# Kernel optimization log

Hardware: AMD Instinct MI355X
Metric: run time of the kernel (lower is better)

Reference implementation:

```python
import jax, jax.numpy as jnp
import numpy as np

ORDER = 2  # kernel_size


def setup_inputs() -> dict:
    key = jax.random.key(0)
    ks = jax.random.split(key, 8)
    B, F, N, T, H = 8, 1, 1024, 128, 64
    c_in = (ORDER * 2 + 1) * (2 * F + H)  # 330
    x = jax.random.normal(ks[0], (B, F, N, T), jnp.float32)
    mask = jax.random.randint(ks[1], (B, F, N, T), 0, 2).astype(jnp.bool_)
    adj = jax.random.uniform(ks[2], (N, N), jnp.float32)
    Wr = jax.random.normal(ks[3], (H, c_in), jnp.float32) * 0.05
    Wu = jax.random.normal(ks[4], (H, c_in), jnp.float32) * 0.05
    Wc = jax.random.normal(ks[5], (H, c_in), jnp.float32) * 0.05
    Wout = jax.random.normal(ks[6], (F, H), jnp.float32) * 0.05
    return {"x": x, "mask": mask, "adj": adj,
            "Wr": Wr, "br": jnp.zeros((H,), jnp.float32),
            "Wu": Wu, "bu": jnp.zeros((H,), jnp.float32),
            "Wc": Wc, "bc": jnp.zeros((H,), jnp.float32),
            "Wout": Wout, "bout": jnp.zeros((F,), jnp.float32)}


def reference(x, mask, adj, Wr, br, Wu, bu, Wc, bc, Wout, bout):
    # compute_support: forward/backward row-normalized diffusion matrices
    sup_f = adj / (adj.sum(1, keepdims=True) + 1e-8)
    adj_t = adj.T
    sup_b = adj_t / (adj_t.sum(1, keepdims=True) + 1e-8)
    supports = (sup_f, sup_b)

    def sconv(z, W, b):  # SpatialConvOrderK, z: [B,C,N]
        outs = [z]
        for a in supports:
            z1 = z
            for _ in range(ORDER):
                z1 = jnp.einsum('bcv,wv->bcw', z1, a)
                outs.append(z1)
        zc = jnp.concatenate(outs, axis=1)  # [B, 5*C, N]
        return jnp.einsum('bcn,oc->bon', zc, W) + b[None, :, None]

    def cell(inp, h):  # GCGRUCell
        xh = jnp.concatenate([inp, h], axis=1)
        r = jax.nn.sigmoid(sconv(xh, Wr, br))
        u = jax.nn.sigmoid(sconv(xh, Wu, bu))
        c = jnp.tanh(sconv(jnp.concatenate([inp, r * h], axis=1), Wc, bc))
        return u * h + (1.0 - u) * c

    B, F, N, T = x.shape
    H = Wout.shape[1]
    h0 = jnp.zeros((B, H, N), x.dtype)  # n_nodes=None -> zero init
    xs = jnp.moveaxis(x, -1, 0)    # [T,B,F,N]
    ms = jnp.moveaxis(mask, -1, 0)

    def step(h, xm):
        x_s, m_s = xm
        x_hat = jnp.einsum('bhn,oh->bon', h, Wout) + bout[None, :, None]
        state = h[None]  # n_layers=1 -> [L,B,H,N]
        x_in = jnp.where(m_s, x_s, x_hat)
        inp = jnp.concatenate([x_in, m_s.astype(x_s.dtype)], axis=1)
        return cell(inp, h), (x_hat, state)

    _, (preds, states) = jax.lax.scan(step, h0, (xs, ms))
    predictions = jnp.moveaxis(preds, 0, -1)  # [B,F,N,T]
    states = jnp.moveaxis(states, 0, -1)      # [L,B,H,N,T]
    return predictions, states
```

## Files before the change

kernel.cpp:

```cpp
#include <hip/hip_runtime.h>
#include <math.h>


typedef unsigned short u16;
typedef unsigned int u32;
typedef short bf16x8 __attribute__((ext_vector_type(8)));
typedef float f32x4 __attribute__((ext_vector_type(4)));

#define MFMA16(a, b, c) __builtin_amdgcn_mfma_f32_16x16x32_bf16((a), (b), (c), 0, 0, 0)

#define Bz 8
#define Tt 128
#define Hh 64
#define KC 416
#define KL 424
#define CP 148
#define ZLB (32 * KL * 2)
#define SCRB (4 * 64 * 44 * 4)

static __device__ __forceinline__ u16 f2b(float f) {
  u32 u = __float_as_uint(f);
  u = (u + 0x7FFFu + ((u >> 16) & 1u)) >> 16;
  return (u16)u;
}
static __device__ __forceinline__ float b2f(u16 s) { return __uint_as_float(((u32)s) << 16); }
static __device__ __forceinline__ bf16x8 ld8(const u16* p) { return *reinterpret_cast<const bf16x8*>(p); }
static __device__ __forceinline__ void st2f(u16* p, float a, float b) {
  *reinterpret_cast<u32*>(p) = (u32)f2b(a) | ((u32)f2b(b) << 16);
}
static __device__ __forceinline__ float sigm(float x) { return 1.f / (1.f + __expf(-x)); }
static __device__ __forceinline__ float tanh_f(float x) {
  x = fminf(fmaxf(x, -15.f), 15.f);
  float e = __expf(2.f * x);
  return (e - 1.f) / (e + 1.f);
}

__global__ __launch_bounds__(256) void ksums(const float* adj, float* rinv, float* cinv) {
  int id = blockIdx.x * 256 + threadIdx.x;
  if (id < 1024) {
    int w = id;
    float s = 0.f;
    for (int v = 0; v < 1024; ++v) s += adj[v * 1024 + w];
    cinv[w] = 1.f / (s + 1e-8f);
  } else {
    int w = id - 1024;
    float s = 0.f;
    for (int v = 0; v < 1024; ++v) s += adj[w * 1024 + v];
    rinv[w] = 1.f / (s + 1e-8f);
  }
}

__global__ __launch_bounds__(256) void kmakeops(const float* adj, const float* rinv, const float* cinv,
                                                u16* Aops, u16* supft, u16* supbt) {
  int idx = blockIdx.x * 256 + threadIdx.x;
  int w = idx >> 10, v = idx & 1023;
  float a = adj[idx];
  u16 f = f2b(a * rinv[w]);
  u16 bb = f2b(a * cinv[v]);
  Aops[idx] = f;
  supft[v * 1024 + w] = f;
  supbt[idx] = bb;
  Aops[2 * 1048576 + v * 1024 + w] = bb;
}

__global__ __launch_bounds__(256) void kA2(u16* Aops, const u16* supft, const u16* supbt) {
  int wg = blockIdx.x;
  int o2 = wg & 1, mt = (wg >> 1) & 7, ntt = (wg >> 4) & 7;
  const u16* Ab = Aops + (o2 ? 2 * 1048576 : 0);
  const u16* Bb = o2 ? supbt : supft;
  u16* Ob = Aops + (o2 ? 3 * 1048576 : 1048576);
  int tid = threadIdx.x, wave = tid >> 6, lane = tid & 63, l15 = lane & 15, quad = lane >> 4;
  int mbase = mt * 128 + wave * 32;
  f32x4 acc[2][8];
#pragma unroll
  for (int m = 0; m < 2; ++m)
#pragma unroll
    for (int j = 0; j < 8; ++j) acc[m][j] = (f32x4){0.f, 0.f, 0.f, 0.f};
  for (int k = 0; k < 1024; k += 32) {
    int kq = k + quad * 8;
    bf16x8 av[2], bv[8];
#pragma unroll
    for (int m = 0; m < 2; ++m) av[m] = ld8(Ab + (mbase + m * 16 + l15) * 1024 + kq);
#pragma unroll
    for (int j = 0; j < 8; ++j) bv[j] = ld8(Bb + (ntt * 128 + j * 16 + l15) * 1024 + kq);
#pragma unroll
    for (int m = 0; m < 2; ++m)
#pragma unroll
      for (int j = 0; j < 8; ++j) acc[m][j] = MFMA16(av[m], bv[j], acc[m][j]);
  }
#pragma unroll
  for (int m = 0; m < 2; ++m)
#pragma unroll
    for (int j = 0; j < 8; ++j) {
      int v = ntt * 128 + j * 16 + l15;
#pragma unroll
      for (int i = 0; i < 4; ++i) {
        int w = mbase + m * 16 + quad * 4 + i;
        Ob[w * 1024 + v] = f2b(acc[m][j][i]);
      }
    }
}

__global__ __launch_bounds__(256) void kpackw(const float* Wr, const float* Wu, const float* Wc,
                                              u16* Wrup, u16* Wcp) {
  int idx = blockIdx.x * 256 + threadIdx.x;
  int r = idx / KC, k = idx % KC;
  if (r >= 192) return;
  float wv = 0.f;
  if (k < 396) {
    int c = (k < 66) ? k : (k - 66);
    if (r < 64) wv = Wr[r * 330 + c];
    else if (r < 128) wv = Wu[(r - 64) * 330 + c];
    else wv = Wc[(r - 128) * 330 + c];
  }
  if (r < 128) Wrup[r * KC + k] = f2b(wv);
  else Wcp[(r - 128) * KC + k] = f2b(wv);
}

__global__ __launch_bounds__(256) void kstep0(const float* x, const int* mask, const float* bout,
                                              float* h, float* states, float* preds,
                                              u16* xh, u16* xc) {
  int wg = blockIdx.x;
  int b = wg / 148, row = wg - b * 148;
  int n = threadIdx.x * 4;
  for (int k = 0; k < 4; ++k, ++n) {
    u16 xhv = 0;
    if (row == 0 || row == 1 || row == 80) {
      int xi = (b * 1024 + n) * 128;
      int mv = mask[xi];
      float xhat = bout[0];
      float xin = mv ? x[xi] : xhat;
      u16 hi = f2b(xin);
      if (row == 0) { xhv = hi; preds[xi] = xhat; }
      else if (row == 1) xhv = f2b((float)mv);
      else xhv = f2b(xin - b2f(hi));
    }
    xh[(b * CP + row) * 1024 + n] = xhv;
    xc[(b * CP + row) * 1024 + n] = 0;
    if (row >= 2 && row < 66) {
      int o = row - 2;
      int idx = (b * 64 + o) * 1024 + n;
      h[idx] = 0.f;
      states[(size_t)idx * 128] = 0.f;
    }
  }
}

__global__ __launch_bounds__(512, 1) void kphA(const u16* __restrict__ xh, const u16* __restrict__ Aops,
                                               const u16* __restrict__ Wrup,
                                               const float* br, const float* bu,
                                               const float* __restrict__ h, float* __restrict__ ubuf,
                                               u16* __restrict__ xc) {
  extern __shared__ char smem[];
  u16 (*zl)[KL] = (u16(*)[KL])smem;
  float* scr = (float*)(smem + ZLB);
  int wg = blockIdx.x;
  int b = wg >> 5, nt = wg & 31;
  int n0 = nt * 32;
  int tid = threadIdx.x, w = tid >> 6, lane = tid & 63, l15 = lane & 15, quad = lane >> 4;
  int op = w & 3, kh = w >> 2;

  for (int i = tid; i < 2112; i += 512) {
    int ch = i >> 4, cp = i & 15;
    int srow = ch < 66 ? ch : ch + 14;
    u32 v = *(const u32*)(xh + (b * CP + srow) * 1024 + n0 + cp * 2);
    zl[cp * 2][ch] = (u16)v;
    zl[cp * 2 + 1][ch] = (u16)(v >> 16);
    if (ch == 0 || ch == 1 || ch == 66 || ch == 67)
      *(u32*)(xc + (b * CP + srow) * 1024 + n0 + cp * 2) = v;
  }
  for (int i = tid; i < 320; i += 512) {
    int n = i / 10, c = i - n * 10;
    ((u32*)zl[n])[198 + c] = 0;
  }

  f32x4 dacc[5][2];
#pragma unroll
  for (int m = 0; m < 5; ++m)
#pragma unroll
    for (int j = 0; j < 2; ++j) dacc[m][j] = (f32x4){0.f, 0.f, 0.f, 0.f};
  {
    const u16* Zb = xh + b * CP * 1024;
    const u16* Ab = Aops + (op << 20);
    int kbase = kh << 9;
    for (int k = 0; k < 512; k += 32) {
      int kq = kbase + k + quad * 8;
      bf16x8 av[5], bv[2];
#pragma unroll
      for (int m = 0; m < 5; ++m) av[m] = ld8(Zb + (m * 16 + l15) * 1024 + kq);
#pragma unroll
      for (int j = 0; j < 2; ++j) bv[j] = ld8(Ab + (n0 + j * 16 + l15) * 1024 + kq);
#pragma unroll
      for (int m = 0; m < 5; ++m)
#pragma unroll
        for (int j = 0; j < 2; ++j) dacc[m][j] = MFMA16(av[m], bv[j], dacc[m][j]);
    }
  }
  if (kh) {
    f32x4* s = (f32x4*)(scr + (op * 64 + lane) * 44);
#pragma unroll
    for (int m = 0; m < 5; ++m)
#pragma unroll
      for (int j = 0; j < 2; ++j) s[m * 2 + j] = dacc[m][j];
  }
  __syncthreads();
  if (!kh) {
    f32x4* s = (f32x4*)(scr + (op * 64 + lane) * 44);
    int cbase = 132 + op * 66;
#pragma unroll
    for (int m = 0; m < 5; ++m)
#pragma unroll
      for (int j = 0; j < 2; ++j) {
        f32x4 a = dacc[m][j] + s[m * 2 + j];
        u16* orow = zl[j * 16 + l15] + cbase;
        int c0 = m * 16 + quad * 4;
        if (c0 < 64) {
          st2f(orow + c0, a[0], a[1]);
          st2f(orow + c0 + 2, a[2], a[3]);
        } else if (c0 == 64) {
          st2f(orow + 64, a[0], a[1]);
        }
      }
  }
  __syncthreads();

  int og = w & 3, obase = og * 32;
  f32x4 cacc[2][2];
#pragma unroll
  for (int m = 0; m < 2; ++m)
#pragma unroll
    for (int j = 0; j < 2; ++j) cacc[m][j] = (f32x4){0.f, 0.f, 0.f, 0.f};
  {
    int k0 = kh ? 224 : 0, k1 = kh ? KC : 224;
    for (int k = k0; k < k1; k += 32) {
      int kq = k + quad * 8;
      bf16x8 av[2], bv[2];
#pragma unroll
      for (int m = 0; m < 2; ++m) av[m] = ld8(Wrup + (obase + m * 16 + l15) * KC + kq);
#pragma unroll
      for (int j = 0; j < 2; ++j) bv[j] = ld8(zl[j * 16 + l15] + kq);
#pragma unroll
      for (int m = 0; m < 2; ++m)
#pragma unroll
        for (int j = 0; j < 2; ++j) cacc[m][j] = MFMA16(av[m], bv[j], cacc[m][j]);
    }
  }
  if (kh) {
    f32x4* s = (f32x4*)(scr + (og * 64 + lane) * 44);
#pragma unroll
    for (int m = 0; m < 2; ++m)
#pragma unroll
      for (int j = 0; j < 2; ++j) s[m * 2 + j] = cacc[m][j];
  }
  __syncthreads();
  if (!kh) {
    f32x4* s = (f32x4*)(scr + (og * 64 + lane) * 44);
#pragma unroll
    for (int m = 0; m < 2; ++m)
#pragma unroll
      for (int j = 0; j < 2; ++j) {
        f32x4 a = cacc[m][j] + s[m * 2 + j];
        int o0 = obase + m * 16 + quad * 4;
        int n = n0 + j * 16 + l15;
        if (o0 < 64) {
#pragma unroll
          for (int i = 0; i < 4; ++i) {
            float sg = sigm(a[i] + br[o0 + i]);
            float rh = sg * h[(b * 64 + o0 + i) * 1024 + n];
            u16 hi = f2b(rh);
            xc[(b * CP + 2 + o0 + i) * 1024 + n] = hi;
            xc[(b * CP + 82 + o0 + i) * 1024 + n] = f2b(rh - b2f(hi));
          }
        } else {
#pragma unroll
          for (int i = 0; i < 4; ++i)
            ubuf[(b * 64 + o0 - 64 + i) * 1024 + n] = sigm(a[i] + bu[o0 - 64 + i]);
        }
      }
  }
}

__global__ __launch_bounds__(512, 1) void kphB(const u16* __restrict__ xc, const u16* __restrict__ Aops,
                                               const u16* __restrict__ Wcp,
                                               const float* bc, const float* __restrict__ ubuf,
                                               float* __restrict__ h, const float* __restrict__ x,
                                               const int* __restrict__ mask, const float* Wout,
                                               const float* bout, float* __restrict__ preds,
                                               float* __restrict__ states, u16* __restrict__ xh,
                                               int t) {
  extern __shared__ char smem[];
  u16 (*yl)[KL] = (u16(*)[KL])smem;
  float* scr = (float*)(smem + ZLB);
  float* hbuf = (float*)(smem + ZLB + SCRB);
  int wg = blockIdx.x;
  int b = wg >> 5, nt = wg & 31;
  int n0 = nt * 32;
  int tid = threadIdx.x, w = tid >> 6, lane = tid & 63, l15 = lane & 15, quad = lane >> 4;
  int op = w & 3, kh = w >> 2;

  for (int i = tid; i < 2112; i += 512) {
    int ch = i >> 4, cp = i & 15;
    int srow = ch < 66 ? ch : ch + 14;
    u32 v = *(const u32*)(xc + (b * CP + srow) * 1024 + n0 + cp * 2);
    yl[cp * 2][ch] = (u16)v;
    yl[cp * 2 + 1][ch] = (u16)(v >> 16);
  }
  for (int i = tid; i < 320; i += 512) {
    int n = i / 10, c = i - n * 10;
    ((u32*)yl[n])[198 + c] = 0;
  }

  f32x4 dacc[5][2];
#pragma unroll
  for (int m = 0; m < 5; ++m)
#pragma unroll
    for (int j = 0; j < 2; ++j) dacc[m][j] = (f32x4){0.f, 0.f, 0.f, 0.f};
  {
    const u16* Zb = xc + b * CP * 1024;
    const u16* Ab = Aops + (op << 20);
    int kbase = kh << 9;
    for (int k = 0; k < 512; k += 32) {
      int kq = kbase + k + quad * 8;
      bf16x8 av[5], bv[2];
#pragma unroll
      for (int m = 0; m < 5; ++m) av[m] = ld8(Zb + (m * 16 + l15) * 1024 + kq);
#pragma unroll
      for (int j = 0; j < 2; ++j) bv[j] = ld8(Ab + (n0 + j * 16 + l15) * 1024 + kq);
#pragma unroll
      for (int m = 0; m < 5; ++m)
#pragma unroll
        for (int j = 0; j < 2; ++j) dacc[m][j] = MFMA16(av[m], bv[j], dacc[m][j]);
    }
  }
  if (kh) {
    f32x4* s = (f32x4*)(scr + (op * 64 + lane) * 44);
#pragma unroll
    for (int m = 0; m < 5; ++m)
#pragma unroll
      for (int j = 0; j < 2; ++j) s[m * 2 + j] = dacc[m][j];
  }
  __syncthreads();
  if (!kh) {
    f32x4* s = (f32x4*)(scr + (op * 64 + lane) * 44);
    int cbase = 132 + op * 66;
#pragma unroll
    for (int m = 0; m < 5; ++m)
#pragma unroll
      for (int j = 0; j < 2; ++j) {
        f32x4 a = dacc[m][j] + s[m * 2 + j];
        u16* orow = yl[j * 16 + l15] + cbase;
        int c0 = m * 16 + quad * 4;
        if (c0 < 64) {
          st2f(orow + c0, a[0], a[1]);
          st2f(orow + c0 + 2, a[2], a[3]);
        } else if (c0 == 64) {
          st2f(orow + 64, a[0], a[1]);
        }
      }
  }
  __syncthreads();

  int og = w & 1, jg = (w >> 1) & 1, task = w & 3;
  int obase = og * 32;
  f32x4 cacc[2];
  cacc[0] = (f32x4){0.f, 0.f, 0.f, 0.f};
  cacc[1] = (f32x4){0.f, 0.f, 0.f, 0.f};
  {
    int k0 = kh ? 224 : 0, k1 = kh ? KC : 224;
    for (int k = k0; k < k1; k += 32) {
      int kq = k + quad * 8;
      bf16x8 bv = ld8(yl[jg * 16 + l15] + kq);
      bf16x8 av0 = ld8(Wcp + (obase + l15) * KC + kq);
      bf16x8 av1 = ld8(Wcp + (obase + 16 + l15) * KC + kq);
      cacc[0] = MFMA16(av0, bv, cacc[0]);
      cacc[1] = MFMA16(av1, bv, cacc[1]);
    }
  }
  if (kh) {
    f32x4* s = (f32x4*)(scr + (task * 64 + lane) * 44);
    s[0] = cacc[0];
    s[1] = cacc[1];
  }
  __syncthreads();
  int t1 = t + 1;
  if (!kh) {
    f32x4* s = (f32x4*)(scr + (task * 64 + lane) * 44);
    int n = n0 + jg * 16 + l15, nloc = jg * 16 + l15;
#pragma unroll
    for (int m = 0; m < 2; ++m) {
      f32x4 a = cacc[m] + s[m];
      int o0 = obase + m * 16 + quad * 4;
#pragma unroll
      for (int i = 0; i < 4; ++i) {
        int o = o0 + i;
        float c = tanh_f(a[i] + bc[o]);
        int idx = (b * 64 + o) * 1024 + n;
        float u = ubuf[idx], hp = h[idx];
        float hn = u * hp + (1.f - u) * c;
        h[idx] = hn;
        hbuf[o * 33 + nloc] = hn;
        u16 hi = f2b(hn);
        if (t1 < Tt) {
          states[(size_t)idx * 128 + t1] = hn;
          xh[(b * CP + 2 + o) * 1024 + n] = hi;
          xh[(b * CP + 82 + o) * 1024 + n] = f2b(hn - b2f(hi));
        }
      }
    }
  }
  __syncthreads();
  if (tid < 32 && t1 < Tt) {
    int nn = n0 + tid;
    float xhat = bout[0];
#pragma unroll
    for (int o = 0; o < 64; ++o) xhat += Wout[o] * hbuf[o * 33 + tid];
    int xi = (b * 1024 + nn) * 128 + t1;
    int mv = mask[xi];
    float xin = mv ? x[xi] : xhat;
    preds[xi] = xhat;
    u16 hi2 = f2b(xin);
    xh[(b * CP + 0) * 1024 + nn] = hi2;
    xh[(b * CP + 1) * 1024 + nn] = f2b((float)mv);
    xh[(b * CP + 80) * 1024 + nn] = f2b(xin - b2f(hi2));
  }
}

extern "C" void kernel_launch(void* const* d_in, const int* in_sizes, int n_in,
                              void* d_out, int out_size, void* d_ws, size_t ws_size,
                              hipStream_t stream) {
  const float* x = (const float*)d_in[0];
  const int* mask = (const int*)d_in[1];
  const float* adj = (const float*)d_in[2];
  const float* Wr = (const float*)d_in[3];
  const float* br = (const float*)d_in[4];
  const float* Wu = (const float*)d_in[5];
  const float* bu = (const float*)d_in[6];
  const float* Wc = (const float*)d_in[7];
  const float* bc = (const float*)d_in[8];
  const float* Wout = (const float*)d_in[9];
  const float* bout = (const float*)d_in[10];

  float* preds = (float*)d_out;
  float* states = preds + 8 * 1024 * 128;

  u16* Aops = (u16*)d_ws;
  u16* supft = Aops + 4 * 1048576;
  u16* supbt = supft + 1048576;
  float* rinv = (float*)(supbt + 1048576);
  float* cinv = rinv + 1024;
  u16* xh = (u16*)(cinv + 1024);
  u16* xc = xh + Bz * CP * 1024;
  u16* Wrup = xc + Bz * CP * 1024;
  u16* Wcp = Wrup + 128 * KC;
  float* ubuf = (float*)(Wcp + 64 * KC);
  float* h = ubuf + Bz * 64 * 1024;

  static int lds_set = 0;
  if (!lds_set) {
    hipFuncSetAttribute((const void*)kphA, hipFuncAttributeMaxDynamicSharedMemorySize, ZLB + SCRB);
    hipFuncSetAttribute((const void*)kphB, hipFuncAttributeMaxDynamicSharedMemorySize,
                        ZLB + SCRB + 64 * 33 * 4);
    lds_set = 1;
  }

  ksums<<<8, 256, 0, stream>>>(adj, rinv, cinv);
  kmakeops<<<4096, 256, 0, stream>>>(adj, rinv, cinv, Aops, supft, supbt);
  kA2<<<128, 256, 0, stream>>>(Aops, supft, supbt);
  kpackw<<<312, 256, 0, stream>>>(Wr, Wu, Wc, Wrup, Wcp);
  kstep0<<<1184, 256, 0, stream>>>(x, mask, bout, h, states, preds, xh, xc);

  for (int t = 0; t < Tt; ++t) {
    kphA<<<256, 512, ZLB + SCRB, stream>>>(xh, Aops, Wrup, br, bu, h, ubuf, xc);
    kphB<<<256, 512, ZLB + SCRB + 64 * 33 * 4, stream>>>(xc, Aops, Wcp, bc, ubuf, h, x, mask,
                                                         Wout, bout, preds, states, xh, t);
  }
}
```

Baseline: 10.09 ms.

## Fuse recurrent timestep loop into one persistent cooperative kernel with grid sync

Replaces the 256 per-step kernel launches with a single cooperative persistent kernel that loops over time and uses grid.sync between phases. Hidden state and the update gate now stay in LDS per workgroup instead of round-tripping through global memory. Global activation buffers shrink to only the rows other blocks need (DP=80), and the lo residual rows are kept local. This removes launch overhead and some global traffic, but adds grid-wide barrier cost and needs all 256 blocks to be co-resident.

```diff
diff --git a/kernel.cpp b/kernel.cpp
--- a/kernel.cpp
+++ b/kernel.cpp
@@ -1,5 +1,8 @@
 #include <hip/hip_runtime.h>
+#include <hip/hip_cooperative_groups.h>
 #include <math.h>
+
+namespace cg = cooperative_groups;
 
 
 typedef unsigned short u16;
@@ -11,12 +14,13 @@
 
 #define Bz 8
 #define Tt 128
-#define Hh 64
 #define KC 416
 #define KL 424
-#define CP 148
+#define DP 80
 #define ZLB (32 * KL * 2)
 #define SCRB (4 * 64 * 44 * 4)
+#define HFB (64 * 33 * 4)
+#define SMEMB (ZLB + SCRB + 2 * HFB + 272)
 
 static __device__ __forceinline__ u16 f2b(float f) {
   u32 u = __float_as_uint(f);
@@ -27,6 +31,9 @@
 static __device__ __forceinline__ bf16x8 ld8(const u16* p) { return *reinterpret_cast<const bf16x8*>(p); }
 static __device__ __forceinline__ void st2f(u16* p, float a, float b) {
   *reinterpret_cast<u32*>(p) = (u32)f2b(a) | ((u32)f2b(b) << 16);
+}
+static __device__ __forceinline__ void st2u(u16* p, u16 a, u16 b) {
+  *reinterpret_cast<u32*>(p) = (u32)a | ((u32)b << 16);
 }
 static __device__ __forceinline__ float sigm(float x) { return 1.f / (1.f + __expf(-x)); }
 static __device__ __forceinline__ float tanh_f(float x) {
@@ -117,311 +124,292 @@
   else Wcp[(r - 128) * KC + k] = f2b(wv);
 }
 
-__global__ __launch_bounds__(256) void kstep0(const float* x, const int* mask, const float* bout,
-                                              float* h, float* states, float* preds,
-                                              u16* xh, u16* xc) {
-  int wg = blockIdx.x;
-  int b = wg / 148, row = wg - b * 148;
-  int n = threadIdx.x * 4;
-  for (int k = 0; k < 4; ++k, ++n) {
-    u16 xhv = 0;
-    if (row == 0 || row == 1 || row == 80) {
-      int xi = (b * 1024 + n) * 128;
-      int mv = mask[xi];
-      float xhat = bout[0];
-      float xin = mv ? x[xi] : xhat;
-      u16 hi = f2b(xin);
-      if (row == 0) { xhv = hi; preds[xi] = xhat; }
-      else if (row == 1) xhv = f2b((float)mv);
-      else xhv = f2b(xin - b2f(hi));
-    }
-    xh[(b * CP + row) * 1024 + n] = xhv;
-    xc[(b * CP + row) * 1024 + n] = 0;
-    if (row >= 2 && row < 66) {
-      int o = row - 2;
-      int idx = (b * 64 + o) * 1024 + n;
-      h[idx] = 0.f;
-      states[(size_t)idx * 128] = 0.f;
-    }
-  }
-}
-
-__global__ __launch_bounds__(512, 1) void kphA(const u16* __restrict__ xh, const u16* __restrict__ Aops,
-                                               const u16* __restrict__ Wrup,
-                                               const float* br, const float* bu,
-                                               const float* __restrict__ h, float* __restrict__ ubuf,
-                                               u16* __restrict__ xc) {
+__global__ __launch_bounds__(512, 1) void kmain(
+    const float* __restrict__ x, const int* __restrict__ mask,
+    const u16* __restrict__ Aops, const u16* __restrict__ Wrup, const u16* __restrict__ Wcp,
+    const float* __restrict__ br, const float* __restrict__ bu, const float* __restrict__ bc,
+    const float* __restrict__ Wout, const float* __restrict__ bout,
+    float* __restrict__ preds, float* __restrict__ states,
+    u16* __restrict__ xhg, u16* __restrict__ xcg) {
   extern __shared__ char smem[];
   u16 (*zl)[KL] = (u16(*)[KL])smem;
   float* scr = (float*)(smem + ZLB);
+  float* hf = (float*)(smem + ZLB + SCRB);
+  float* uf = (float*)(smem + ZLB + SCRB + HFB);
+  float* wsh = (float*)(smem + ZLB + SCRB + 2 * HFB);
+
+  cg::grid_group grid = cg::this_grid();
   int wg = blockIdx.x;
-  int b = wg >> 5, nt = wg & 31;
-  int n0 = nt * 32;
+  int b = wg >> 5, nt = wg & 31, n0 = nt * 32;
   int tid = threadIdx.x, w = tid >> 6, lane = tid & 63, l15 = lane & 15, quad = lane >> 4;
   int op = w & 3, kh = w >> 2;
 
-  for (int i = tid; i < 2112; i += 512) {
-    int ch = i >> 4, cp = i & 15;
-    int srow = ch < 66 ? ch : ch + 14;
-    u32 v = *(const u32*)(xh + (b * CP + srow) * 1024 + n0 + cp * 2);
-    zl[cp * 2][ch] = (u16)v;
-    zl[cp * 2 + 1][ch] = (u16)(v >> 16);
-    if (ch == 0 || ch == 1 || ch == 66 || ch == 67)
-      *(u32*)(xc + (b * CP + srow) * 1024 + n0 + cp * 2) = v;
-  }
-  for (int i = tid; i < 320; i += 512) {
-    int n = i / 10, c = i - n * 10;
-    ((u32*)zl[n])[198 + c] = 0;
-  }
-
-  f32x4 dacc[5][2];
-#pragma unroll
-  for (int m = 0; m < 5; ++m)
-#pragma unroll
-    for (int j = 0; j < 2; ++j) dacc[m][j] = (f32x4){0.f, 0.f, 0.f, 0.f};
-  {
-    const u16* Zb = xh + b * CP * 1024;
-    const u16* Ab = Aops + (op << 20);
-    int kbase = kh << 9;
-    for (int k = 0; k < 512; k += 32) {
-      int kq = kbase + k + quad * 8;
-      bf16x8 av[5], bv[2];
-#pragma unroll
-      for (int m = 0; m < 5; ++m) av[m] = ld8(Zb + (m * 16 + l15) * 1024 + kq);
-#pragma unroll
-      for (int j = 0; j < 2; ++j) bv[j] = ld8(Ab + (n0 + j * 16 + l15) * 1024 + kq);
-#pragma unroll
-      for (int m = 0; m < 5; ++m)
-#pragma unroll
-        for (int j = 0; j < 2; ++j) dacc[m][j] = MFMA16(av[m], bv[j], dacc[m][j]);
-    }
-  }
-  if (kh) {
-    f32x4* s = (f32x4*)(scr + (op * 64 + lane) * 44);
-#pragma unroll
-    for (int m = 0; m < 5; ++m)
-#pragma unroll
-      for (int j = 0; j < 2; ++j) s[m * 2 + j] = dacc[m][j];
+  for (int i = tid; i < 6784; i += 512) ((u32*)smem)[i] = 0;
+  for (int i = tid; i < 4224; i += 512) hf[i] = 0.f;
+  if (tid < 64) wsh[tid] = Wout[tid];
+  if (tid == 64) wsh[64] = bout[0];
+  for (int i = tid; i < 1280; i += 512) {
+    int row = i >> 4, cp = i & 15;
+    int a = (b * DP + row) * 1024 + n0 + cp * 2;
+    *(u32*)(xhg + a) = 0;
+    *(u32*)(xcg + a) = 0;
+  }
+  for (int i = tid; i < 2048; i += 512) {
+    int o = i >> 5, nn = i & 31;
+    states[(size_t)((b * 64 + o) * 1024 + n0 + nn) * 128] = 0.f;
   }
   __syncthreads();
-  if (!kh) {
-    f32x4* s = (f32x4*)(scr + (op * 64 + lane) * 44);
-    int cbase = 132 + op * 66;
-#pragma unroll
-    for (int m = 0; m < 5; ++m)
-#pragma unroll
-      for (int j = 0; j < 2; ++j) {
-        f32x4 a = dacc[m][j] + s[m * 2 + j];
-        u16* orow = zl[j * 16 + l15] + cbase;
-        int c0 = m * 16 + quad * 4;
-        if (c0 < 64) {
-          st2f(orow + c0, a[0], a[1]);
-          st2f(orow + c0 + 2, a[2], a[3]);
-        } else if (c0 == 64) {
-          st2f(orow + 64, a[0], a[1]);
-        }
-      }
-  }
-  __syncthreads();
-
-  int og = w & 3, obase = og * 32;
-  f32x4 cacc[2][2];
-#pragma unroll
-  for (int m = 0; m < 2; ++m)
-#pragma unroll
-    for (int j = 0; j < 2; ++j) cacc[m][j] = (f32x4){0.f, 0.f, 0.f, 0.f};
-  {
-    int k0 = kh ? 224 : 0, k1 = kh ? KC : 224;
-    for (int k = k0; k < k1; k += 32) {
-      int kq = k + quad * 8;
-      bf16x8 av[2], bv[2];
-#pragma unroll
-      for (int m = 0; m < 2; ++m) av[m] = ld8(Wrup + (obase + m * 16 + l15) * KC + kq);
-#pragma unroll
-      for (int j = 0; j < 2; ++j) bv[j] = ld8(zl[j * 16 + l15] + kq);
-#pragma unroll
-      for (int m = 0; m < 2; ++m)
-#pragma unroll
-        for (int j = 0; j < 2; ++j) cacc[m][j] = MFMA16(av[m], bv[j], cacc[m][j]);
-    }
-  }
-  if (kh) {
-    f32x4* s = (f32x4*)(scr + (og * 64 + lane) * 44);
-#pragma unroll
-    for (int m = 0; m < 2; ++m)
-#pragma unroll
-      for (int j = 0; j < 2; ++j) s[m * 2 + j] = cacc[m][j];
-  }
-  __syncthreads();
-  if (!kh) {
-    f32x4* s = (f32x4*)(scr + (og * 64 + lane) * 44);
-#pragma unroll
-    for (int m = 0; m < 2; ++m)
-#pragma unroll
-      for (int j = 0; j < 2; ++j) {
-        f32x4 a = cacc[m][j] + s[m * 2 + j];
-        int o0 = obase + m * 16 + quad * 4;
-        int n = n0 + j * 16 + l15;
-        if (o0 < 64) {
-#pragma unroll
-          for (int i = 0; i < 4; ++i) {
-            float sg = sigm(a[i] + br[o0 + i]);
-            float rh = sg * h[(b * 64 + o0 + i) * 1024 + n];
-            u16 hi = f2b(rh);
-            xc[(b * CP + 2 + o0 + i) * 1024 + n] = hi;
-            xc[(b * CP + 82 + o0 + i) * 1024 + n] = f2b(rh - b2f(hi));
-          }
-        } else {
-#pragma unroll
-          for (int i = 0; i < 4; ++i)
-            ubuf[(b * 64 + o0 - 64 + i) * 1024 + n] = sigm(a[i] + bu[o0 - 64 + i]);
-        }
-      }
-  }
-}
-
-__global__ __launch_bounds__(512, 1) void kphB(const u16* __restrict__ xc, const u16* __restrict__ Aops,
-                                               const u16* __restrict__ Wcp,
-                                               const float* bc, const float* __restrict__ ubuf,
-                                               float* __restrict__ h, const float* __restrict__ x,
-                                               const int* __restrict__ mask, const float* Wout,
-                                               const float* bout, float* __restrict__ preds,
-                                               float* __restrict__ states, u16* __restrict__ xh,
-                                               int t) {
-  extern __shared__ char smem[];
-  u16 (*yl)[KL] = (u16(*)[KL])smem;
-  float* scr = (float*)(smem + ZLB);
-  float* hbuf = (float*)(smem + ZLB + SCRB);
-  int wg = blockIdx.x;
-  int b = wg >> 5, nt = wg & 31;
-  int n0 = nt * 32;
-  int tid = threadIdx.x, w = tid >> 6, lane = tid & 63, l15 = lane & 15, quad = lane >> 4;
-  int op = w & 3, kh = w >> 2;
-
-  for (int i = tid; i < 2112; i += 512) {
-    int ch = i >> 4, cp = i & 15;
-    int srow = ch < 66 ? ch : ch + 14;
-    u32 v = *(const u32*)(xc + (b * CP + srow) * 1024 + n0 + cp * 2);
-    yl[cp * 2][ch] = (u16)v;
-    yl[cp * 2 + 1][ch] = (u16)(v >> 16);
-  }
-  for (int i = tid; i < 320; i += 512) {
-    int n = i / 10, c = i - n * 10;
-    ((u32*)yl[n])[198 + c] = 0;
-  }
-
-  f32x4 dacc[5][2];
-#pragma unroll
-  for (int m = 0; m < 5; ++m)
-#pragma unroll
-    for (int j = 0; j < 2; ++j) dacc[m][j] = (f32x4){0.f, 0.f, 0.f, 0.f};
-  {
-    const u16* Zb = xc + b * CP * 1024;
-    const u16* Ab = Aops + (op << 20);
-    int kbase = kh << 9;
-    for (int k = 0; k < 512; k += 32) {
-      int kq = kbase + k + quad * 8;
-      bf16x8 av[5], bv[2];
-#pragma unroll
-      for (int m = 0; m < 5; ++m) av[m] = ld8(Zb + (m * 16 + l15) * 1024 + kq);
-#pragma unroll
-      for (int j = 0; j < 2; ++j) bv[j] = ld8(Ab + (n0 + j * 16 + l15) * 1024 + kq);
-#pragma unroll
-      for (int m = 0; m < 5; ++m)
-#pragma unroll
-        for (int j = 0; j < 2; ++j) dacc[m][j] = MFMA16(av[m], bv[j], dacc[m][j]);
-    }
-  }
-  if (kh) {
-    f32x4* s = (f32x4*)(scr + (op * 64 + lane) * 44);
-#pragma unroll
-    for (int m = 0; m < 5; ++m)
-#pragma unroll
-      for (int j = 0; j < 2; ++j) s[m * 2 + j] = dacc[m][j];
-  }
-  __syncthreads();
-  if (!kh) {
-    f32x4* s = (f32x4*)(scr + (op * 64 + lane) * 44);
-    int cbase = 132 + op * 66;
-#pragma unroll
-    for (int m = 0; m < 5; ++m)
-#pragma unroll
-      for (int j = 0; j < 2; ++j) {
-        f32x4 a = dacc[m][j] + s[m * 2 + j];
-        u16* orow = yl[j * 16 + l15] + cbase;
-        int c0 = m * 16 + quad * 4;
-        if (c0 < 64) {
-          st2f(orow + c0, a[0], a[1]);
-          st2f(orow + c0 + 2, a[2], a[3]);
-        } else if (c0 == 64) {
-          st2f(orow + 64, a[0], a[1]);
-        }
-      }
-  }
-  __syncthreads();
-
-  int og = w & 1, jg = (w >> 1) & 1, task = w & 3;
-  int obase = og * 32;
-  f32x4 cacc[2];
-  cacc[0] = (f32x4){0.f, 0.f, 0.f, 0.f};
-  cacc[1] = (f32x4){0.f, 0.f, 0.f, 0.f};
-  {
-    int k0 = kh ? 224 : 0, k1 = kh ? KC : 224;
-    for (int k = k0; k < k1; k += 32) {
-      int kq = k + quad * 8;
-      bf16x8 bv = ld8(yl[jg * 16 + l15] + kq);
-      bf16x8 av0 = ld8(Wcp + (obase + l15) * KC + kq);
-      bf16x8 av1 = ld8(Wcp + (obase + 16 + l15) * KC + kq);
-      cacc[0] = MFMA16(av0, bv, cacc[0]);
-      cacc[1] = MFMA16(av1, bv, cacc[1]);
-    }
-  }
-  if (kh) {
-    f32x4* s = (f32x4*)(scr + (task * 64 + lane) * 44);
-    s[0] = cacc[0];
-    s[1] = cacc[1];
-  }
-  __syncthreads();
-  int t1 = t + 1;
-  if (!kh) {
-    f32x4* s = (f32x4*)(scr + (task * 64 + lane) * 44);
-    int n = n0 + jg * 16 + l15, nloc = jg * 16 + l15;
-#pragma unroll
-    for (int m = 0; m < 2; ++m) {
-      f32x4 a = cacc[m] + s[m];
-      int o0 = obase + m * 16 + quad * 4;
-#pragma unroll
-      for (int i = 0; i < 4; ++i) {
-        int o = o0 + i;
-        float c = tanh_f(a[i] + bc[o]);
-        int idx = (b * 64 + o) * 1024 + n;
-        float u = ubuf[idx], hp = h[idx];
-        float hn = u * hp + (1.f - u) * c;
-        h[idx] = hn;
-        hbuf[o * 33 + nloc] = hn;
-        u16 hi = f2b(hn);
-        if (t1 < Tt) {
-          states[(size_t)idx * 128 + t1] = hn;
-          xh[(b * CP + 2 + o) * 1024 + n] = hi;
-          xh[(b * CP + 82 + o) * 1024 + n] = f2b(hn - b2f(hi));
-        }
-      }
-    }
-  }
-  __syncthreads();
-  if (tid < 32 && t1 < Tt) {
+  if (tid < 32) {
     int nn = n0 + tid;
-    float xhat = bout[0];
-#pragma unroll
-    for (int o = 0; o < 64; ++o) xhat += Wout[o] * hbuf[o * 33 + tid];
-    int xi = (b * 1024 + nn) * 128 + t1;
+    int xi = (b * 1024 + nn) * 128;
+    float xhat = wsh[64];
     int mv = mask[xi];
     float xin = mv ? x[xi] : xhat;
     preds[xi] = xhat;
-    u16 hi2 = f2b(xin);
-    xh[(b * CP + 0) * 1024 + nn] = hi2;
-    xh[(b * CP + 1) * 1024 + nn] = f2b((float)mv);
-    xh[(b * CP + 80) * 1024 + nn] = f2b(xin - b2f(hi2));
+    u16 hi = f2b(xin), lo = f2b(xin - b2f(hi)), mb = f2b((float)mv);
+    zl[tid][0] = hi; zl[tid][1] = mb; zl[tid][66] = lo;
+    xhg[(b * DP + 0) * 1024 + nn] = hi;
+    xhg[(b * DP + 1) * 1024 + nn] = mb;
+    xcg[(b * DP + 0) * 1024 + nn] = hi;
+    xcg[(b * DP + 1) * 1024 + nn] = mb;
+  }
+  __threadfence();
+  grid.sync();
+
+  for (int t = 0; t < Tt - 1; ++t) {
+    int t1 = t + 1;
+    {
+      f32x4 dacc[5][2];
+#pragma unroll
+      for (int m = 0; m < 5; ++m)
+#pragma unroll
+        for (int j = 0; j < 2; ++j) dacc[m][j] = (f32x4){0.f, 0.f, 0.f, 0.f};
+      {
+        const u16* Zb = xhg + b * DP * 1024;
+        const u16* Ab = Aops + (op << 20);
+        int kbase = kh << 9;
+        for (int k = 0; k < 512; k += 32) {
+          int kq = kbase + k + quad * 8;
+          bf16x8 av[5], bv[2];
+#pragma unroll
+          for (int m = 0; m < 5; ++m) av[m] = ld8(Zb + (m * 16 + l15) * 1024 + kq);
+#pragma unroll
+          for (int j = 0; j < 2; ++j) bv[j] = ld8(Ab + (n0 + j * 16 + l15) * 1024 + kq);
+#pragma unroll
+          for (int m = 0; m < 5; ++m)
+#pragma unroll
+            for (int j = 0; j < 2; ++j) dacc[m][j] = MFMA16(av[m], bv[j], dacc[m][j]);
+        }
+      }
+      if (kh) {
+        f32x4* s = (f32x4*)(scr + (op * 64 + lane) * 44);
+#pragma unroll
+        for (int m = 0; m < 5; ++m)
+#pragma unroll
+          for (int j = 0; j < 2; ++j) s[m * 2 + j] = dacc[m][j];
+      }
+      __syncthreads();
+      if (!kh) {
+        f32x4* s = (f32x4*)(scr + (op * 64 + lane) * 44);
+        int cbase = 132 + op * 66;
+#pragma unroll
+        for (int m = 0; m < 5; ++m)
+#pragma unroll
+          for (int j = 0; j < 2; ++j) {
+            f32x4 a = dacc[m][j] + s[m * 2 + j];
+            u16* orow = zl[j * 16 + l15] + cbase;
+            int c0 = m * 16 + quad * 4;
+            if (c0 < 64) {
+              st2f(orow + c0, a[0], a[1]);
+              st2f(orow + c0 + 2, a[2], a[3]);
+            } else if (c0 == 64) {
+              st2f(orow + 64, a[0], a[1]);
+            }
+          }
+      }
+      __syncthreads();
+
+      int og = op, obase = og * 32;
+      f32x4 cacc[2][2];
+#pragma unroll
+      for (int m = 0; m < 2; ++m)
+#pragma unroll
+        for (int j = 0; j < 2; ++j) cacc[m][j] = (f32x4){0.f, 0.f, 0.f, 0.f};
+      {
+        int k0 = kh ? 224 : 0, k1 = kh ? KC : 224;
+        for (int k = k0; k < k1; k += 32) {
+          int kq = k + quad * 8;
+          bf16x8 av[2], bv[2];
+#pragma unroll
+          for (int m = 0; m < 2; ++m) av[m] = ld8(Wrup + (obase + m * 16 + l15) * KC + kq);
+#pragma unroll
+          for (int j = 0; j < 2; ++j) bv[j] = ld8(zl[j * 16 + l15] + kq);
+#pragma unroll
+          for (int m = 0; m < 2; ++m)
+#pragma unroll
+            for (int j = 0; j < 2; ++j) cacc[m][j] = MFMA16(av[m], bv[j], cacc[m][j]);
+        }
+      }
+      if (kh) {
+        f32x4* s = (f32x4*)(scr + (og * 64 + lane) * 44);
+#pragma unroll
+        for (int m = 0; m < 2; ++m)
+#pragma unroll
+          for (int j = 0; j < 2; ++j) s[m * 2 + j] = cacc[m][j];
+      }
+      __syncthreads();
+      if (!kh) {
+        f32x4* s = (f32x4*)(scr + (og * 64 + lane) * 44);
+#pragma unroll
+        for (int m = 0; m < 2; ++m)
+#pragma unroll
+          for (int j = 0; j < 2; ++j) {
+            f32x4 a = cacc[m][j] + s[m * 2 + j];
+            int o0 = obase + m * 16 + quad * 4;
+            int nl = j * 16 + l15, n = n0 + nl;
+            if (o0 < 64) {
+              u16 hi4[4], lo4[4];
+#pragma unroll
+              for (int i = 0; i < 4; ++i) {
+                float sg = sigm(a[i] + br[o0 + i]);
+                float rh = sg * hf[(o0 + i) * 33 + nl];
+                hi4[i] = f2b(rh);
+                lo4[i] = f2b(rh - b2f(hi4[i]));
+                xcg[(b * DP + 2 + o0 + i) * 1024 + n] = hi4[i];
+              }
+              st2u(&zl[nl][2 + o0], hi4[0], hi4[1]);
+              st2u(&zl[nl][4 + o0], hi4[2], hi4[3]);
+              st2u(&zl[nl][68 + o0], lo4[0], lo4[1]);
+              st2u(&zl[nl][70 + o0], lo4[2], lo4[3]);
+            } else {
+#pragma unroll
+              for (int i = 0; i < 4; ++i)
+                uf[(o0 - 64 + i) * 33 + nl] = sigm(a[i] + bu[o0 - 64 + i]);
+            }
+          }
+      }
+      __threadfence();
+      grid.sync();
+    }
+    {
+      f32x4 dacc[5][2];
+#pragma unroll
+      for (int m = 0; m < 5; ++m)
+#pragma unroll
+        for (int j = 0; j < 2; ++j) dacc[m][j] = (f32x4){0.f, 0.f, 0.f, 0.f};
+      {
+        const u16* Zb = xcg + b * DP * 1024;
+        const u16* Ab = Aops + (op << 20);
+        int kbase = kh << 9;
+        for (int k = 0; k < 512; k += 32) {
+          int kq = kbase + k + quad * 8;
+          bf16x8 av[5], bv[2];
+#pragma unroll
+          for (int m = 0; m < 5; ++m) av[m] = ld8(Zb + (m * 16 + l15) * 1024 + kq);
+#pragma unroll
+          for (int j = 0; j < 2; ++j) bv[j] = ld8(Ab + (n0 + j * 16 + l15) * 1024 + kq);
+#pragma unroll
+          for (int m = 0; m < 5; ++m)
+#pragma unroll
+            for (int j = 0; j < 2; ++j) dacc[m][j] = MFMA16(av[m], bv[j], dacc[m][j]);
+        }
+      }
+      if (kh) {
+        f32x4* s = (f32x4*)(scr + (op * 64 + lane) * 44);
+#pragma unroll
+        for (int m = 0; m < 5; ++m)
+#pragma unroll
+          for (int j = 0; j < 2; ++j) s[m * 2 + j] = dacc[m][j];
+      }
+      __syncthreads();
+      if (!kh) {
+        f32x4* s = (f32x4*)(scr + (op * 64 + lane) * 44);
+        int cbase = 132 + op * 66;
+#pragma unroll
+        for (int m = 0; m < 5; ++m)
+#pragma unroll
+          for (int j = 0; j < 2; ++j) {
+            f32x4 a = dacc[m][j] + s[m * 2 + j];
+            u16* orow = zl[j * 16 + l15] + cbase;
+            int c0 = m * 16 + quad * 4;
+            if (c0 < 64) {
+              st2f(orow + c0, a[0], a[1]);
+              st2f(orow + c0 + 2, a[2], a[3]);
+            } else if (c0 == 64) {
+              st2f(orow + 64, a[0], a[1]);
+            }
+          }
+      }
+      __syncthreads();
+
+      int og = w & 1, jg = (w >> 1) & 1, task = w & 3;
+      int obase = og * 32;
+      f32x4 cacc[2];
+      cacc[0] = (f32x4){0.f, 0.f, 0.f, 0.f};
+      cacc[1] = (f32x4){0.f, 0.f, 0.f, 0.f};
+      {
+        int k0 = kh ? 224 : 0, k1 = kh ? KC : 224;
+        for (int k = k0; k < k1; k += 32) {
+          int kq = k + quad * 8;
+          bf16x8 bv = ld8(zl[jg * 16 + l15] + kq);
+          bf16x8 av0 = ld8(Wcp + (obase + l15) * KC + kq);
+          bf16x8 av1 = ld8(Wcp + (obase + 16 + l15) * KC + kq);
+          cacc[0] = MFMA16(av0, bv, cacc[0]);
+          cacc[1] = MFMA16(av1, bv, cacc[1]);
+        }
+      }
+      if (kh) {
+        f32x4* s = (f32x4*)(scr + (task * 64 + lane) * 44);
+        s[0] = cacc[0];
+        s[1] = cacc[1];
+      }
+      __syncthreads();
+      if (!kh) {
+        f32x4* s = (f32x4*)(scr + (task * 64 + lane) * 44);
+        int nl = jg * 16 + l15, n = n0 + nl;
+#pragma unroll
+        for (int m = 0; m < 2; ++m) {
+          f32x4 a = cacc[m] + s[m];
+          int o0 = obase + m * 16 + quad * 4;
+          u16 hi4[4], lo4[4];
+#pragma unroll
+          for (int i = 0; i < 4; ++i) {
+            int o = o0 + i;
+            float c = tanh_f(a[i] + bc[o]);
+            float u = uf[o * 33 + nl], hp = hf[o * 33 + nl];
+            float hn = u * hp + (1.f - u) * c;
+            hf[o * 33 + nl] = hn;
+            hi4[i] = f2b(hn);
+            lo4[i] = f2b(hn - b2f(hi4[i]));
+            states[(size_t)((b * 64 + o) * 1024 + n) * 128 + t1] = hn;
+            xhg[(b * DP + 2 + o) * 1024 + n] = hi4[i];
+          }
+          st2u(&zl[nl][2 + o0], hi4[0], hi4[1]);
+          st2u(&zl[nl][4 + o0], hi4[2], hi4[3]);
+          st2u(&zl[nl][68 + o0], lo4[0], lo4[1]);
+          st2u(&zl[nl][70 + o0], lo4[2], lo4[3]);
+        }
+      }
+      __syncthreads();
+      if (tid < 32) {
+        int nn = n0 + tid;
+        float xhat = wsh[64];
+#pragma unroll
+        for (int o = 0; o < 64; ++o) xhat += wsh[o] * hf[o * 33 + tid];
+        int xi = (b * 1024 + nn) * 128 + t1;
+        int mv = mask[xi];
+        float xin = mv ? x[xi] : xhat;
+        preds[xi] = xhat;
+        u16 hi2 = f2b(xin), lo2 = f2b(xin - b2f(hi2)), mb = f2b((float)mv);
+        zl[tid][0] = hi2; zl[tid][1] = mb; zl[tid][66] = lo2;
+        xhg[(b * DP + 0) * 1024 + nn] = hi2;
+        xhg[(b * DP + 1) * 1024 + nn] = mb;
+        xcg[(b * DP + 0) * 1024 + nn] = hi2;
+        xcg[(b * DP + 1) * 1024 + nn] = mb;
+      }
+      __threadfence();
+      grid.sync();
+    }
   }
 }
 
@@ -448,18 +436,14 @@
   u16* supbt = supft + 1048576;
   float* rinv = (float*)(supbt + 1048576);
   float* cinv = rinv + 1024;
-  u16* xh = (u16*)(cinv + 1024);
-  u16* xc = xh + Bz * CP * 1024;
-  u16* Wrup = xc + Bz * CP * 1024;
+  u16* xhg = (u16*)(cinv + 1024);
+  u16* xcg = xhg + Bz * DP * 1024;
+  u16* Wrup = xcg + Bz * DP * 1024;
   u16* Wcp = Wrup + 128 * KC;
-  float* ubuf = (float*)(Wcp + 64 * KC);
-  float* h = ubuf + Bz * 64 * 1024;
 
   static int lds_set = 0;
   if (!lds_set) {
-    hipFuncSetAttribute((const void*)kphA, hipFuncAttributeMaxDynamicSharedMemorySize, ZLB + SCRB);
-    hipFuncSetAttribute((const void*)kphB, hipFuncAttributeMaxDynamicSharedMemorySize,
-                        ZLB + SCRB + 64 * 33 * 4);
+    hipFuncSetAttribute((const void*)kmain, hipFuncAttributeMaxDynamicSharedMemorySize, SMEMB);
     lds_set = 1;
   }
 
@@ -467,11 +451,9 @@
   kmakeops<<<4096, 256, 0, stream>>>(adj, rinv, cinv, Aops, supft, supbt);
   kA2<<<128, 256, 0, stream>>>(Aops, supft, supbt);
   kpackw<<<312, 256, 0, stream>>>(Wr, Wu, Wc, Wrup, Wcp);
-  kstep0<<<1184, 256, 0, stream>>>(x, mask, bout, h, states, preds, xh, xc);
-
-  for (int t = 0; t < Tt; ++t) {
-    kphA<<<256, 512, ZLB + SCRB, stream>>>(xh, Aops, Wrup, br, bu, h, ubuf, xc);
-    kphB<<<256, 512, ZLB + SCRB + 64 * 33 * 4, stream>>>(xc, Aops, Wcp, bc, ubuf, h, x, mask,
-                                                         Wout, bout, preds, states, xh, t);
-  }
-}
+
+  void* args[] = {(void*)&x, (void*)&mask, (void*)&Aops, (void*)&Wrup, (void*)&Wcp,
+                  (void*)&br, (void*)&bu, (void*)&bc, (void*)&Wout, (void*)&bout,
+                  (void*)&preds, (void*)&states, (void*)&xhg, (void*)&xcg};
+  hipLaunchCooperativeKernel((void*)kmain, dim3(256), dim3(512), args, SMEMB, stream);
+}
```

Result: slower. 30.10 ms (+198.4%).
